# Kernel tuning notes

Hardware: AMD Instinct MI355X
Metric: run time of the kernel (lower is better)

Reference implementation:

```python
import jax, jax.numpy as jnp
import numpy as np

N, E, H = 50000, 800000, 4
IN_C, HID, OUT = 256, 64, 64
NEG_SLOPE = 0.2   # PyG GATConv default leaky_relu slope
EPS_BN = 1e-5
EPS_SM = 1e-16    # PyG softmax denominator eps


def setup_inputs() -> dict:
    key = jax.random.key(0)
    ks = jax.random.split(key, 16)
    inp = {
        "x": jax.random.normal(ks[0], (N, IN_C), jnp.float32),
        "edge_index": jax.random.randint(ks[1], (2, E), 0, N, jnp.int32),
    }
    dims = [(IN_C, HID), (HID, HID), (HID, OUT)]
    j = 2
    for l, (di, do) in enumerate(dims):
        s = 1.0 / np.sqrt(di)
        inp[f"W{l}"] = jax.random.normal(ks[j], (di, H * do), jnp.float32) * s; j += 1
        inp[f"as{l}"] = jax.random.normal(ks[j], (H, do), jnp.float32) * 0.1; j += 1
        inp[f"ad{l}"] = jax.random.normal(ks[j], (H, do), jnp.float32) * 0.1; j += 1
        inp[f"b{l}"] = jnp.zeros((do,), jnp.float32)
    for l in range(2):  # BN after all but the last conv
        inp[f"g{l}"] = jnp.ones((HID,), jnp.float32)
        inp[f"be{l}"] = jnp.zeros((HID,), jnp.float32)
    return inp


def _gat_layer(x, src, dst, W, a_src, a_dst, bias):
    """PyG GATConv, heads=H, concat=False (mean over heads), add_self_loops already in src/dst."""
    n = x.shape[0]
    C = a_src.shape[1]
    h = (x @ W).reshape(n, H, C)                      # [N,H,C]
    a_l = jnp.einsum('nhc,hc->nh', h, a_src)          # src attention term per node
    a_r = jnp.einsum('nhc,hc->nh', h, a_dst)          # dst attention term per node
    e = jax.nn.leaky_relu(a_l[src] + a_r[dst], NEG_SLOPE)   # [E',H]
    # segment softmax over incoming edges of each dst node
    m = jax.ops.segment_max(e, dst, num_segments=n)
    m = jnp.where(jnp.isfinite(m), m, 0.0)
    p = jnp.exp(e - m[dst])
    den = jax.ops.segment_sum(p, dst, num_segments=n)
    alpha = p / (den[dst] + EPS_SM)                   # [E',H]
    msg = h[src] * alpha[:, :, None]                  # [E',H,C]
    out = jax.ops.segment_sum(msg, dst, num_segments=n)
    return out.mean(axis=1) + bias                    # concat=False -> head mean, then bias


def _bn(x, g, b):
    # BatchNorm1d training-mode statistics (biased variance), eps=1e-5
    mu = x.mean(axis=0)
    var = x.var(axis=0)
    return (x - mu) * jax.lax.rsqrt(var + EPS_BN) * g + b


def reference(x, edge_index, W0, as0, ad0, b0, W1, as1, ad1, b1,
              W2, as2, ad2, b2, g0, be0, g1, be1):
    n = x.shape[0]
    loops = jnp.arange(n, dtype=edge_index.dtype)
    src = jnp.concatenate([edge_index[0], loops])
    dst = jnp.concatenate([edge_index[1], loops])

    h = _gat_layer(x, src, dst, W0, as0, ad0, b0)
    h = jax.nn.relu(_bn(h, g0, be0))                  # dropout: eval mode (identity)
    h = _gat_layer(h, src, dst, W1, as1, ad1, b1)
    h = jax.nn.relu(_bn(h, g1, be1))
    out = _gat_layer(h, src, dst, W2, as2, ad2, b2)
    return out
```

## Files before the change

### kernel.cpp

```cpp
#include <hip/hip_runtime.h>
#include <hip/hip_fp16.h>
#include <math.h>

constexpr float NEG_SLOPE = 0.2f;
constexpr float EPS_BN = 1e-5f;
constexpr float EPS_SM = 1e-16f;

typedef _Float16 half8 __attribute__((ext_vector_type(8)));
typedef float f32x4 __attribute__((ext_vector_type(4)));

__device__ __forceinline__ float lrelu(float x){ return x >= 0.f ? x : NEG_SLOPE * x; }

__global__ void k_init(int* cnt, int n, float* bn, int* tick){
  int i = blockIdx.x * blockDim.x + threadIdx.x;
  if (i < n) cnt[i] = 0;
  if (i < 256) bn[i] = 0.f;
  if (i < 4) tick[i] = 0;
}

__global__ void k_convW3(const float* __restrict__ W0, const float* __restrict__ W1,
                         const float* __restrict__ W2, _Float16* __restrict__ Wt0,
                         _Float16* __restrict__ Wt1, _Float16* __restrict__ Wt2){
  int t = blockIdx.x * blockDim.x + threadIdx.x;
  if (t < 65536){
    int n = t & 255, k = t >> 8;
    Wt0[(size_t)n * 256 + k] = (_Float16)W0[(size_t)k * 256 + n];
  } else if (t < 81920){
    int u = t - 65536; int n = u & 255, k = u >> 8;
    Wt1[(size_t)n * 64 + k] = (_Float16)W1[(size_t)k * 256 + n];
  } else if (t < 98304){
    int u = t - 81920; int n = u & 255, k = u >> 8;
    Wt2[(size_t)n * 64 + k] = (_Float16)W2[(size_t)k * 256 + n];
  }
}

__global__ void k_count(const int* __restrict__ ei, int E, int N, int* __restrict__ cnt){
  int e = blockIdx.x * blockDim.x + threadIdx.x;
  if (e >= E + N) return;
  int dst = (e < E) ? ei[E + e] : (e - E);
  atomicAdd(&cnt[dst], 1);
}

__global__ __launch_bounds__(256) void k_blocksum(const int* __restrict__ cnt, int n, int chunk,
                                                  int* __restrict__ part){
  __shared__ int s[256];
  int b = blockIdx.x, t = threadIdx.x;
  int lo = b * chunk, hi = min(n, lo + chunk);
  int v = 0;
  for (int i = lo + t; i < hi; i += 256) v += cnt[i];
  s[t] = v;
  __syncthreads();
  #pragma unroll
  for (int off = 128; off > 0; off >>= 1){
    if (t < off) s[t] += s[t + off];
    __syncthreads();
  }
  if (t == 0) part[b] = s[0];
}

__global__ __launch_bounds__(256) void k_scanpart(int* __restrict__ part, int* __restrict__ ptr, int n){
  __shared__ int s[256];
  int t = threadIdx.x;
  int v = part[t];
  s[t] = v;
  __syncthreads();
  #pragma unroll
  for (int off = 1; off < 256; off <<= 1){
    int u = (t >= off) ? s[t - off] : 0;
    __syncthreads();
    s[t] += u;
    __syncthreads();
  }
  part[t] = s[t] - v;
  if (t == 255) ptr[n] = s[255];
}

__global__ __launch_bounds__(256) void k_localscan(const int* __restrict__ cnt, const int* __restrict__ part,
                                                   int n, int chunk, int* __restrict__ ptr,
                                                   int* __restrict__ cursor){
  __shared__ int s[256];
  int b = blockIdx.x, t = threadIdx.x;
  int i = b * chunk + t;
  int v = (t < chunk && i < n) ? cnt[i] : 0;
  s[t] = v;
  __syncthreads();
  #pragma unroll
  for (int off = 1; off < 256; off <<= 1){
    int u = (t >= off) ? s[t - off] : 0;
    __syncthreads();
    s[t] += u;
    __syncthreads();
  }
  if (t < chunk && i < n){
    int ex = part[b] + s[t] - v;
    ptr[i] = ex;
    cursor[i] = ex;
  }
}

__global__ void k_fill(const int* __restrict__ ei, int E, int N,
                       int* __restrict__ cursor, int* __restrict__ csr_src){
  int e = blockIdx.x * blockDim.x + threadIdx.x;
  if (e >= E + N) return;
  int src, dst;
  if (e < E){ src = ei[e]; dst = ei[E + e]; } else { src = e - E; dst = e - E; }
  int slot = atomicAdd(&cursor[dst], 1);
  csr_src[slot] = src;
}

__global__ __launch_bounds__(256) void k_gemm(const float* __restrict__ X,
    const _Float16* __restrict__ Wt, const float* __restrict__ a_s, const float* __restrict__ a_d,
    __half* __restrict__ hb, float* __restrict__ al, float* __restrict__ ar, int nrows, int K,
    const float* __restrict__ scale, const float* __restrict__ shift){
  __shared__ _Float16 Alds[4][128][8];
  __shared__ _Float16 Blds[4][64][8];
  int tid = threadIdx.x;
  int m0 = blockIdx.x * 128;
  int head = blockIdx.y;
  int n0 = head * 64;
  int w = tid >> 6, l = tid & 63;
  int lm = l & 15, lq = l >> 4;
  int qs = tid & 3, rs = tid >> 2;
  f32x4 acc[2][4] = {};

  for (int k0 = 0; k0 < K; k0 += 32){
    float4 sc0, sc1, sh0, sh1;
    if (scale){
      sc0 = *(const float4*)(scale + k0 + qs * 8);
      sc1 = *(const float4*)(scale + k0 + qs * 8 + 4);
      sh0 = *(const float4*)(shift + k0 + qs * 8);
      sh1 = *(const float4*)(shift + k0 + qs * 8 + 4);
    }
    #pragma unroll
    for (int it = 0; it < 2; it++){
      int row = it * 64 + rs;
      int gr = m0 + row;
      float4 v0 = make_float4(0,0,0,0), v1 = make_float4(0,0,0,0);
      if (gr < nrows){
        v0 = *(const float4*)(X + (size_t)gr * K + k0 + qs * 8);
        v1 = *(const float4*)(X + (size_t)gr * K + k0 + qs * 8 + 4);
      }
      if (scale){
        v0.x = fmaxf(fmaf(v0.x, sc0.x, sh0.x), 0.f);
        v0.y = fmaxf(fmaf(v0.y, sc0.y, sh0.y), 0.f);
        v0.z = fmaxf(fmaf(v0.z, sc0.z, sh0.z), 0.f);
        v0.w = fmaxf(fmaf(v0.w, sc0.w, sh0.w), 0.f);
        v1.x = fmaxf(fmaf(v1.x, sc1.x, sh1.x), 0.f);
        v1.y = fmaxf(fmaf(v1.y, sc1.y, sh1.y), 0.f);
        v1.z = fmaxf(fmaf(v1.z, sc1.z, sh1.z), 0.f);
        v1.w = fmaxf(fmaf(v1.w, sc1.w, sh1.w), 0.f);
      }
      half8 h = {(_Float16)v0.x, (_Float16)v0.y, (_Float16)v0.z, (_Float16)v0.w,
                 (_Float16)v1.x, (_Float16)v1.y, (_Float16)v1.z, (_Float16)v1.w};
      *(half8*)&Alds[qs][row][0] = h;
    }
    *(half8*)&Blds[qs][rs][0] = *(const half8*)(Wt + (size_t)(n0 + rs) * K + k0 + qs * 8);
    __syncthreads();
    half8 af0 = *(const half8*)&Alds[lq][w * 32 + lm][0];
    half8 af1 = *(const half8*)&Alds[lq][w * 32 + 16 + lm][0];
    #pragma unroll
    for (int nt = 0; nt < 4; nt++){
      half8 bf = *(const half8*)&Blds[lq][nt * 16 + lm][0];
      acc[0][nt] = __builtin_amdgcn_mfma_f32_16x16x32_f16(af0, bf, acc[0][nt], 0, 0, 0);
      acc[1][nt] = __builtin_amdgcn_mfma_f32_16x16x32_f16(af1, bf, acc[1][nt], 0, 0, 0);
    }
    __syncthreads();
  }

  float asv[4], adv[4];
  #pragma unroll
  for (int nt = 0; nt < 4; nt++){
    asv[nt] = a_s[n0 + nt * 16 + lm];
    adv[nt] = a_d[n0 + nt * 16 + lm];
  }
  #pragma unroll
  for (int s = 0; s < 2; s++){
    #pragma unroll
    for (int reg = 0; reg < 4; reg++){
      float sl = 0.f, sr = 0.f;
      #pragma unroll
      for (int nt = 0; nt < 4; nt++){
        sl += acc[s][nt][reg] * asv[nt];
        sr += acc[s][nt][reg] * adv[nt];
      }
      #pragma unroll
      for (int off = 1; off < 16; off <<= 1){
        sl += __shfl_xor(sl, off);
        sr += __shfl_xor(sr, off);
      }
      int grow = m0 + w * 32 + s * 16 + lq * 4 + reg;
      if (lm == 0 && grow < nrows){
        al[(size_t)grow * 4 + head] = sl;
        ar[(size_t)grow * 4 + head] = sr;
      }
    }
  }
  #pragma unroll
  for (int s = 0; s < 2; s++){
    #pragma unroll
    for (int nt = 0; nt < 4; nt++){
      #pragma unroll
      for (int reg = 0; reg < 4; reg++){
        int grow = m0 + w * 32 + s * 16 + lq * 4 + reg;
        if (grow < nrows)
          hb[(size_t)grow * 256 + n0 + nt * 16 + lm] = __float2half(acc[s][nt][reg]);
      }
    }
  }
}

__global__ __launch_bounds__(256) void k_node(const int* __restrict__ ptr,
    const int* __restrict__ csr, const __half* __restrict__ hb,
    const float* __restrict__ al, const float* __restrict__ ar,
    const float* __restrict__ bias, float* __restrict__ out, int N){
  __shared__ int2 ssw[4][64][4];
  int n = (blockIdx.x * blockDim.x + threadIdx.x) >> 6;
  int lane = threadIdx.x & 63;
  int wv = threadIdx.x >> 6;
  if (n >= N) return;
  int beg = ptr[n], end = ptr[n + 1];
  int deg = end - beg;
  float4 arv = *(const float4*)(ar + (size_t)n * 4);
  int hd = lane >> 4;
  int cg = (lane & 15) * 4;
  const __half* hbase = hb + hd * 64 + cg;
  float ax = 0.f, ay = 0.f, az = 0.f, aw = 0.f;

  if (deg <= 64){
    int idx = beg + lane;
    bool act = idx < end;
    int mye = act ? csr[idx] : 0;
    float e0 = -1e30f, e1 = -1e30f, e2 = -1e30f, e3 = -1e30f;
    if (act){
      float4 av = *(const float4*)(al + (size_t)mye * 4);
      e0 = lrelu(av.x + arv.x); e1 = lrelu(av.y + arv.y);
      e2 = lrelu(av.z + arv.z); e3 = lrelu(av.w + arv.w);
    }
    float m0 = e0, m1 = e1, m2 = e2, m3 = e3;
    #pragma unroll
    for (int off = 32; off > 0; off >>= 1){
      m0 = fmaxf(m0, __shfl_xor(m0, off));
      m1 = fmaxf(m1, __shfl_xor(m1, off));
      m2 = fmaxf(m2, __shfl_xor(m2, off));
      m3 = fmaxf(m3, __shfl_xor(m3, off));
    }
    float w0 = __expf(e0 - m0), w1 = __expf(e1 - m1);
    float w2 = __expf(e2 - m2), w3 = __expf(e3 - m3);
    float d0 = w0, d1 = w1, d2 = w2, d3 = w3;
    #pragma unroll
    for (int off = 32; off > 0; off >>= 1){
      d0 += __shfl_xor(d0, off);
      d1 += __shfl_xor(d1, off);
      d2 += __shfl_xor(d2, off);
      d3 += __shfl_xor(d3, off);
    }
    int4* wr = (int4*)&ssw[wv][lane][0];
    wr[0] = make_int4(mye, __float_as_int(w0 / (d0 + EPS_SM)),
                      mye, __float_as_int(w1 / (d1 + EPS_SM)));
    wr[1] = make_int4(mye, __float_as_int(w2 / (d2 + EPS_SM)),
                      mye, __float_as_int(w3 / (d3 + EPS_SM)));
    __builtin_amdgcn_wave_barrier();
    const int2* phd = &ssw[wv][0][hd];
    #pragma unroll 4
    for (int j = 0; j < deg; j++){
      int2 sw = phd[j * 4];
      float w = __int_as_float(sw.y);
      ushort4 u = *(const ushort4*)(hbase + (size_t)sw.x * 256);
      ax = fmaf(__half2float(__ushort_as_half(u.x)), w, ax);
      ay = fmaf(__half2float(__ushort_as_half(u.y)), w, ay);
      az = fmaf(__half2float(__ushort_as_half(u.z)), w, az);
      aw = fmaf(__half2float(__ushort_as_half(u.w)), w, aw);
    }
  } else {
    float m0 = -1e30f, m1 = -1e30f, m2 = -1e30f, m3 = -1e30f;
    for (int i = beg + lane; i < end; i += 64){
      int s = csr[i];
      float4 av = *(const float4*)(al + (size_t)s * 4);
      m0 = fmaxf(m0, lrelu(av.x + arv.x));
      m1 = fmaxf(m1, lrelu(av.y + arv.y));
      m2 = fmaxf(m2, lrelu(av.z + arv.z));
      m3 = fmaxf(m3, lrelu(av.w + arv.w));
    }
    #pragma unroll
    for (int off = 32; off > 0; off >>= 1){
      m0 = fmaxf(m0, __shfl_xor(m0, off));
      m1 = fmaxf(m1, __shfl_xor(m1, off));
      m2 = fmaxf(m2, __shfl_xor(m2, off));
      m3 = fmaxf(m3, __shfl_xor(m3, off));
    }
    float d0 = 0.f, d1 = 0.f, d2 = 0.f, d3 = 0.f;
    for (int i = beg + lane; i < end; i += 64){
      int s = csr[i];
      float4 av = *(const float4*)(al + (size_t)s * 4);
      d0 += __expf(lrelu(av.x + arv.x) - m0);
      d1 += __expf(lrelu(av.y + arv.y) - m1);
      d2 += __expf(lrelu(av.z + arv.z) - m2);
      d3 += __expf(lrelu(av.w + arv.w) - m3);
    }
    #pragma unroll
    for (int off = 32; off > 0; off >>= 1){
      d0 += __shfl_xor(d0, off);
      d1 += __shfl_xor(d1, off);
      d2 += __shfl_xor(d2, off);
      d3 += __shfl_xor(d3, off);
    }
    float i0 = 1.f / (d0 + EPS_SM), i1 = 1.f / (d1 + EPS_SM);
    float i2 = 1.f / (d2 + EPS_SM), i3 = 1.f / (d3 + EPS_SM);
    float arh = hd == 0 ? arv.x : hd == 1 ? arv.y : hd == 2 ? arv.z : arv.w;
    float mh  = hd == 0 ? m0 : hd == 1 ? m1 : hd == 2 ? m2 : m3;
    float ih  = hd == 0 ? i0 : hd == 1 ? i1 : hd == 2 ? i2 : i3;
    for (int i = beg; i < end; i++){
      int s = csr[i];
      float w = __expf(lrelu(al[(size_t)s * 4 + hd] + arh) - mh) * ih;
      ushort4 u = *(const ushort4*)(hbase + (size_t)s * 256);
      ax = fmaf(__half2float(__ushort_as_half(u.x)), w, ax);
      ay = fmaf(__half2float(__ushort_as_half(u.y)), w, ay);
      az = fmaf(__half2float(__ushort_as_half(u.z)), w, az);
      aw = fmaf(__half2float(__ushort_as_half(u.w)), w, aw);
    }
  }

  #pragma unroll
  for (int off = 16; off <= 32; off <<= 1){
    ax += __shfl_xor(ax, off);
    ay += __shfl_xor(ay, off);
    az += __shfl_xor(az, off);
    aw += __shfl_xor(aw, off);
  }
  if (lane < 16){
    float4 b4 = *(const float4*)(bias + cg);
    *(float4*)(out + (size_t)n * 64 + cg) =
        make_float4(ax * 0.25f + b4.x, ay * 0.25f + b4.y, az * 0.25f + b4.z, aw * 0.25f + b4.w);
  }
}

__global__ __launch_bounds__(256) void k_bnstats(const float* __restrict__ x, int N,
                                                 float* __restrict__ gsum, float* __restrict__ gsq,
                                                 int* __restrict__ tick,
                                                 const float* __restrict__ g, const float* __restrict__ be,
                                                 float* __restrict__ scale, float* __restrict__ shift){
  int c = threadIdx.x & 63;
  int rg = threadIdx.x >> 6;
  float s = 0.f, q = 0.f;
  for (int r = blockIdx.x * 4 + rg; r < N; r += gridDim.x * 4){
    float v = x[(size_t)r * 64 + c];
    s += v; q += v * v;
  }
  __shared__ float ls[4][64], lq[4][64];
  __shared__ int amLast;
  ls[rg][c] = s; lq[rg][c] = q;
  __syncthreads();
  if (rg == 0){
    s = ls[0][c] + ls[1][c] + ls[2][c] + ls[3][c];
    q = lq[0][c] + lq[1][c] + lq[2][c] + lq[3][c];
    atomicAdd(&gsum[c], s);
    atomicAdd(&gsq[c], q);
  }
  __threadfence();
  if (threadIdx.x == 0)
    amLast = (atomicAdd(tick, 1) == (int)gridDim.x - 1) ? 1 : 0;
  __syncthreads();
  if (amLast && threadIdx.x < 64){
    float gs = atomicAdd(&gsum[c], 0.f);
    float gq = atomicAdd(&gsq[c], 0.f);
    float m = gs / (float)N;
    float v = gq / (float)N - m * m;
    float sc = g[c] * rsqrtf(v + EPS_BN);
    scale[c] = sc;
    shift[c] = be[c] - m * sc;
  }
}

extern "C" void kernel_launch(void* const* d_in, const int* in_sizes, int n_in,
                              void* d_out, int out_size, void* d_ws, size_t ws_size,
                              hipStream_t stream){
  const float* x  = (const float*)d_in[0];
  const int*   ei = (const int*)d_in[1];
  const float* W[3]  = {(const float*)d_in[2], (const float*)d_in[6],  (const float*)d_in[10]};
  const float* AS[3] = {(const float*)d_in[3], (const float*)d_in[7],  (const float*)d_in[11]};
  const float* AD[3] = {(const float*)d_in[4], (const float*)d_in[8],  (const float*)d_in[12]};
  const float* BI[3] = {(const float*)d_in[5], (const float*)d_in[9],  (const float*)d_in[13]};
  const float* G[2]  = {(const float*)d_in[14], (const float*)d_in[16]};
  const float* BE[2] = {(const float*)d_in[15], (const float*)d_in[17]};
  const int N = in_sizes[0] / 256;
  const int E = in_sizes[1] / 2;
  const int EN = E + N;

  char* wsb = (char*)d_ws;
  size_t off = 0;
  auto alloc = [&](size_t bytes) -> char* {
    char* p = wsb + off;
    off = (off + bytes + 255) & ~(size_t)255;
    return p;
  };
  int* cnt      = (int*)alloc((size_t)N * 4);
  int* cursor   = (int*)alloc((size_t)N * 4);
  int* rowptr   = (int*)alloc((size_t)(N + 1) * 4);
  int* part     = (int*)alloc(256 * 4);
  int* csr      = (int*)alloc((size_t)EN * 4);
  _Float16* Wt0 = (_Float16*)alloc((size_t)256 * 256 * 2);
  _Float16* Wt1 = (_Float16*)alloc((size_t)64 * 256 * 2);
  _Float16* Wt2 = (_Float16*)alloc((size_t)64 * 256 * 2);
  __half* hb    = (__half*)alloc((size_t)N * 256 * 2);
  float* al     = (float*)alloc((size_t)N * 4 * 4);
  float* ar     = (float*)alloc((size_t)N * 4 * 4);
  float* bufA   = (float*)alloc((size_t)N * 64 * 4);
  float* bn     = (float*)alloc(256 * 4);
  int*   tick   = (int*)alloc(4 * 4);
  float* murs   = (float*)alloc(128 * 4);

  const int chunk = (N + 255) / 256;

  k_init<<<(N + 255) / 256, 256, 0, stream>>>(cnt, N, bn, tick);
  k_count<<<(EN + 255) / 256, 256, 0, stream>>>(ei, E, N, cnt);
  k_blocksum<<<256, 256, 0, stream>>>(cnt, N, chunk, part);
  k_scanpart<<<1, 256, 0, stream>>>(part, rowptr, N);
  k_localscan<<<256, 256, 0, stream>>>(cnt, part, N, chunk, rowptr, cursor);
  k_fill<<<(EN + 255) / 256, 256, 0, stream>>>(ei, E, N, cursor, csr);
  k_convW3<<<384, 256, 0, stream>>>(W[0], W[1], W[2], Wt0, Wt1, Wt2);

  const _Float16* Wt[3] = {Wt0, Wt1, Wt2};
  const float* lin = x;
  for (int l = 0; l < 3; l++){
    int K = (l == 0) ? 256 : 64;
    const float* sc = (l == 0) ? nullptr : murs;
    const float* sh = (l == 0) ? nullptr : murs + 64;
    dim3 gg((N + 127) / 128, 4);
    k_gemm<<<gg, 256, 0, stream>>>(lin, Wt[l], AS[l], AD[l], hb, al, ar, N, K, sc, sh);
    float* outp = (l == 2) ? (float*)d_out : bufA;
    k_node<<<(N + 3) / 4, 256, 0, stream>>>(rowptr, csr, hb, al, ar, BI[l], outp, N);
    if (l < 2){
      float* gsum = bn + l * 128;
      float* gsq  = gsum + 64;
      k_bnstats<<<128, 256, 0, stream>>>(bufA, N, gsum, gsq, tick + l, G[l], BE[l], murs, murs + 64);
      lin = bufA;
    }
  }
}
```

Measured before the change: 555.5 us.

## Compute all four heads per GEMM block and fuse setup kernels

The GEMM now covers all 256 output columns (four heads) in one block, with each wave owning one head. The grid drops its head dimension, so each X tile is loaded and BN-transformed once instead of four times. The init and weight-conversion kernels are merged into one launch, and the block-sum and partial-scan kernels are merged using a last-block atomic ticket. In exchange the GEMM holds 32 accumulator tiles per thread and uses a larger LDS buffer, which raises register pressure and may lower occupancy; launch_bounds(256,2) is added to limit this.

```diff
diff --git a/kernel.cpp b/kernel.cpp
--- a/kernel.cpp
+++ b/kernel.cpp
@@ -11,26 +11,23 @@
 
 __device__ __forceinline__ float lrelu(float x){ return x >= 0.f ? x : NEG_SLOPE * x; }
 
-__global__ void k_init(int* cnt, int n, float* bn, int* tick){
-  int i = blockIdx.x * blockDim.x + threadIdx.x;
-  if (i < n) cnt[i] = 0;
-  if (i < 256) bn[i] = 0.f;
-  if (i < 4) tick[i] = 0;
-}
-
-__global__ void k_convW3(const float* __restrict__ W0, const float* __restrict__ W1,
-                         const float* __restrict__ W2, _Float16* __restrict__ Wt0,
-                         _Float16* __restrict__ Wt1, _Float16* __restrict__ Wt2){
+__global__ void k_prep(int* cnt, int n, float* bn, int* tick,
+                       const float* __restrict__ W0, const float* __restrict__ W1,
+                       const float* __restrict__ W2, _Float16* __restrict__ Wt0,
+                       _Float16* __restrict__ Wt1, _Float16* __restrict__ Wt2){
   int t = blockIdx.x * blockDim.x + threadIdx.x;
+  if (t < n) cnt[t] = 0;
+  if (t < 256) bn[t] = 0.f;
+  if (t < 4) tick[t] = 0;
   if (t < 65536){
-    int n = t & 255, k = t >> 8;
-    Wt0[(size_t)n * 256 + k] = (_Float16)W0[(size_t)k * 256 + n];
+    int c = t & 255, k = t >> 8;
+    Wt0[(size_t)c * 256 + k] = (_Float16)W0[(size_t)k * 256 + c];
   } else if (t < 81920){
-    int u = t - 65536; int n = u & 255, k = u >> 8;
-    Wt1[(size_t)n * 64 + k] = (_Float16)W1[(size_t)k * 256 + n];
+    int u = t - 65536; int c = u & 255, k = u >> 8;
+    Wt1[(size_t)c * 64 + k] = (_Float16)W1[(size_t)k * 256 + c];
   } else if (t < 98304){
-    int u = t - 81920; int n = u & 255, k = u >> 8;
-    Wt2[(size_t)n * 64 + k] = (_Float16)W2[(size_t)k * 256 + n];
+    int u = t - 81920; int c = u & 255, k = u >> 8;
+    Wt2[(size_t)c * 64 + k] = (_Float16)W2[(size_t)k * 256 + c];
   }
 }
 
@@ -41,9 +38,11 @@
   atomicAdd(&cnt[dst], 1);
 }
 
-__global__ __launch_bounds__(256) void k_blocksum(const int* __restrict__ cnt, int n, int chunk,
-                                                  int* __restrict__ part){
+__global__ __launch_bounds__(256) void k_bsumscan(const int* __restrict__ cnt, int n, int chunk,
+                                                  int* __restrict__ part, int* __restrict__ ptr,
+                                                  int* __restrict__ tick){
   __shared__ int s[256];
+  __shared__ int amLast;
   int b = blockIdx.x, t = threadIdx.x;
   int lo = b * chunk, hi = min(n, lo + chunk);
   int v = 0;
@@ -56,23 +55,23 @@
     __syncthreads();
   }
   if (t == 0) part[b] = s[0];
-}
-
-__global__ __launch_bounds__(256) void k_scanpart(int* __restrict__ part, int* __restrict__ ptr, int n){
-  __shared__ int s[256];
-  int t = threadIdx.x;
-  int v = part[t];
-  s[t] = v;
+  __threadfence();
+  if (t == 0) amLast = (atomicAdd(tick, 1) == (int)gridDim.x - 1) ? 1 : 0;
   __syncthreads();
-  #pragma unroll
-  for (int off = 1; off < 256; off <<= 1){
-    int u = (t >= off) ? s[t - off] : 0;
-    __syncthreads();
-    s[t] += u;
-    __syncthreads();
-  }
-  part[t] = s[t] - v;
-  if (t == 255) ptr[n] = s[255];
+  if (amLast){
+    int pv = atomicAdd(&part[t], 0);
+    s[t] = pv;
+    __syncthreads();
+    #pragma unroll
+    for (int off = 1; off < 256; off <<= 1){
+      int u = (t >= off) ? s[t - off] : 0;
+      __syncthreads();
+      s[t] += u;
+      __syncthreads();
+    }
+    part[t] = s[t] - pv;
+    if (t == 255) ptr[n] = s[255];
+  }
 }
 
 __global__ __launch_bounds__(256) void k_localscan(const int* __restrict__ cnt, const int* __restrict__ part,
@@ -108,20 +107,18 @@
   csr_src[slot] = src;
 }
 
-__global__ __launch_bounds__(256) void k_gemm(const float* __restrict__ X,
+__global__ __launch_bounds__(256, 2) void k_gemm(const float* __restrict__ X,
     const _Float16* __restrict__ Wt, const float* __restrict__ a_s, const float* __restrict__ a_d,
     __half* __restrict__ hb, float* __restrict__ al, float* __restrict__ ar, int nrows, int K,
     const float* __restrict__ scale, const float* __restrict__ shift){
-  __shared__ _Float16 Alds[4][128][8];
-  __shared__ _Float16 Blds[4][64][8];
+  __shared__ _Float16 Alds[4][129][8];
+  __shared__ _Float16 Blds[4][257][8];
   int tid = threadIdx.x;
   int m0 = blockIdx.x * 128;
-  int head = blockIdx.y;
-  int n0 = head * 64;
   int w = tid >> 6, l = tid & 63;
   int lm = l & 15, lq = l >> 4;
   int qs = tid & 3, rs = tid >> 2;
-  f32x4 acc[2][4] = {};
+  f32x4 acc[8][4] = {};
 
   for (int k0 = 0; k0 < K; k0 += 32){
     float4 sc0, sc1, sh0, sh1;
@@ -154,56 +151,57 @@
                  (_Float16)v1.x, (_Float16)v1.y, (_Float16)v1.z, (_Float16)v1.w};
       *(half8*)&Alds[qs][row][0] = h;
     }
-    *(half8*)&Blds[qs][rs][0] = *(const half8*)(Wt + (size_t)(n0 + rs) * K + k0 + qs * 8);
-    __syncthreads();
-    half8 af0 = *(const half8*)&Alds[lq][w * 32 + lm][0];
-    half8 af1 = *(const half8*)&Alds[lq][w * 32 + 16 + lm][0];
-    #pragma unroll
-    for (int nt = 0; nt < 4; nt++){
-      half8 bf = *(const half8*)&Blds[lq][nt * 16 + lm][0];
-      acc[0][nt] = __builtin_amdgcn_mfma_f32_16x16x32_f16(af0, bf, acc[0][nt], 0, 0, 0);
-      acc[1][nt] = __builtin_amdgcn_mfma_f32_16x16x32_f16(af1, bf, acc[1][nt], 0, 0, 0);
+    #pragma unroll
+    for (int it = 0; it < 4; it++){
+      int col = it * 64 + rs;
+      *(half8*)&Blds[qs][col][0] = *(const half8*)(Wt + (size_t)col * K + k0 + qs * 8);
+    }
+    __syncthreads();
+    half8 af[8];
+    #pragma unroll
+    for (int mf = 0; mf < 8; mf++) af[mf] = *(const half8*)&Alds[lq][mf * 16 + lm][0];
+    #pragma unroll
+    for (int j = 0; j < 4; j++){
+      half8 bf = *(const half8*)&Blds[lq][(w * 4 + j) * 16 + lm][0];
+      #pragma unroll
+      for (int mf = 0; mf < 8; mf++)
+        acc[mf][j] = __builtin_amdgcn_mfma_f32_16x16x32_f16(af[mf], bf, acc[mf][j], 0, 0, 0);
     }
     __syncthreads();
   }
 
   float asv[4], adv[4];
   #pragma unroll
-  for (int nt = 0; nt < 4; nt++){
-    asv[nt] = a_s[n0 + nt * 16 + lm];
-    adv[nt] = a_d[n0 + nt * 16 + lm];
+  for (int j = 0; j < 4; j++){
+    asv[j] = a_s[w * 64 + j * 16 + lm];
+    adv[j] = a_d[w * 64 + j * 16 + lm];
   }
   #pragma unroll
-  for (int s = 0; s < 2; s++){
+  for (int mf = 0; mf < 8; mf++){
     #pragma unroll
     for (int reg = 0; reg < 4; reg++){
-      float sl = 0.f, sr = 0.f;
-      #pragma unroll
-      for (int nt = 0; nt < 4; nt++){
-        sl += acc[s][nt][reg] * asv[nt];
-        sr += acc[s][nt][reg] * adv[nt];
-      }
+      float sl = acc[mf][0][reg] * asv[0] + acc[mf][1][reg] * asv[1]
+               + acc[mf][2][reg] * asv[2] + acc[mf][3][reg] * asv[3];
+      float sr = acc[mf][0][reg] * adv[0] + acc[mf][1][reg] * adv[1]
+               + acc[mf][2][reg] * adv[2] + acc[mf][3][reg] * adv[3];
       #pragma unroll
       for (int off = 1; off < 16; off <<= 1){
         sl += __shfl_xor(sl, off);
         sr += __shfl_xor(sr, off);
       }
-      int grow = m0 + w * 32 + s * 16 + lq * 4 + reg;
-      if (lm == 0 && grow < nrows){
-        al[(size_t)grow * 4 + head] = sl;
-        ar[(size_t)grow * 4 + head] = sr;
+      int row = m0 + mf * 16 + lq * 4 + reg;
+      if (lm == 0 && row < nrows){
+        al[(size_t)row * 4 + w] = sl;
+        ar[(size_t)row * 4 + w] = sr;
       }
     }
-  }
-  #pragma unroll
-  for (int s = 0; s < 2; s++){
-    #pragma unroll
-    for (int nt = 0; nt < 4; nt++){
+    #pragma unroll
+    for (int j = 0; j < 4; j++){
       #pragma unroll
       for (int reg = 0; reg < 4; reg++){
-        int grow = m0 + w * 32 + s * 16 + lq * 4 + reg;
-        if (grow < nrows)
-          hb[(size_t)grow * 256 + n0 + nt * 16 + lm] = __float2half(acc[s][nt][reg]);
+        int row = m0 + mf * 16 + lq * 4 + reg;
+        if (row < nrows)
+          hb[(size_t)row * 256 + w * 64 + j * 16 + lm] = __float2half(acc[mf][j][reg]);
       }
     }
   }
@@ -411,13 +409,11 @@
 
   const int chunk = (N + 255) / 256;
 
-  k_init<<<(N + 255) / 256, 256, 0, stream>>>(cnt, N, bn, tick);
+  k_prep<<<384, 256, 0, stream>>>(cnt, N, bn, tick, W[0], W[1], W[2], Wt0, Wt1, Wt2);
   k_count<<<(EN + 255) / 256, 256, 0, stream>>>(ei, E, N, cnt);
-  k_blocksum<<<256, 256, 0, stream>>>(cnt, N, chunk, part);
-  k_scanpart<<<1, 256, 0, stream>>>(part, rowptr, N);
+  k_bsumscan<<<256, 256, 0, stream>>>(cnt, N, chunk, part, rowptr, tick + 2);
   k_localscan<<<256, 256, 0, stream>>>(cnt, part, N, chunk, rowptr, cursor);
   k_fill<<<(EN + 255) / 256, 256, 0, stream>>>(ei, E, N, cursor, csr);
-  k_convW3<<<384, 256, 0, stream>>>(W[0], W[1], W[2], Wt0, Wt1, Wt2);
 
   const _Float16* Wt[3] = {Wt0, Wt1, Wt2};
   const float* lin = x;
@@ -425,8 +421,7 @@
     int K = (l == 0) ? 256 : 64;
     const float* sc = (l == 0) ? nullptr : murs;
     const float* sh = (l == 0) ? nullptr : murs + 64;
-    dim3 gg((N + 127) / 128, 4);
-    k_gemm<<<gg, 256, 0, stream>>>(lin, Wt[l], AS[l], AD[l], hb, al, ar, N, K, sc, sh);
+    k_gemm<<<(N + 127) / 128, 256, 0, stream>>>(lin, Wt[l], AS[l], AD[l], hb, al, ar, N, K, sc, sh);
     float* outp = (l == 2) ? (float*)d_out : bufA;
     k_node<<<(N + 3) / 4, 256, 0, stream>>>(rowptr, csr, hb, al, ar, BI[l], outp, N);
     if (l < 2){
```

Result: no change. 559.3 us (+0.7%).
